# Kernel optimization log

Hardware: AMD Instinct MI355X
Metric: run time of the kernel (lower is better)

The kernel has to match this reference:

```python
import jax, jax.numpy as jnp
import numpy as np

H = 128  # rnn_size

def _run_lstm(x, Wih, Whh, bih, bhh):
    # x: [B, T, D]; Wih: [4H, D]; Whh: [4H, H]; biases: [4H]
    B = x.shape[0]
    xg = jnp.einsum('btd,gd->btg', x, Wih) + bih + bhh  # precompute input projection [B,T,4H]
    WhhT = Whh.T  # [H, 4H]
    def step(carry, xg_t):
        h, c = carry
        g = xg_t + h @ WhhT  # [B, 4H]
        i = jax.nn.sigmoid(g[:, :H])
        f = jax.nn.sigmoid(g[:, H:2 * H])
        gg = jnp.tanh(g[:, 2 * H:3 * H])
        o = jax.nn.sigmoid(g[:, 3 * H:])
        c = f * c + i * gg
        h = o * jnp.tanh(c)
        return (h, c), h
    init = (jnp.zeros((B, H), x.dtype), jnp.zeros((B, H), x.dtype))
    _, ys = jax.lax.scan(step, init, jnp.swapaxes(xg, 0, 1))  # [T, B, H]
    return jnp.swapaxes(ys, 0, 1)  # [B, T, H]

def _bilstm(x, layers):
    h = x
    for (fw, bw) in layers:
        yf = _run_lstm(h, *fw)
        yb = jnp.flip(_run_lstm(jnp.flip(h, axis=1), *bw), axis=1)
        h = jnp.concatenate([yf, yb], axis=-1)  # [B, T, 2H]
    return h

def setup_inputs() -> dict:
    key = jax.random.key(0)
    ks = iter(jax.random.split(key, 32))
    B, T, D = 64, 512, 64
    s = 0.08  # init scale ~ 1/sqrt(H) to avoid gate saturation
    inp = {'x': jax.random.normal(next(ks), (B, T, D), jnp.float32)}
    for name, shape in [
        ('Wih00', (4 * H, D)), ('Whh00', (4 * H, H)), ('bih00', (4 * H,)), ('bhh00', (4 * H,)),
        ('Wih01', (4 * H, D)), ('Whh01', (4 * H, H)), ('bih01', (4 * H,)), ('bhh01', (4 * H,)),
        ('Wih10', (4 * H, 2 * H)), ('Whh10', (4 * H, H)), ('bih10', (4 * H,)), ('bhh10', (4 * H,)),
        ('Wih11', (4 * H, 2 * H)), ('Whh11', (4 * H, H)), ('bih11', (4 * H,)), ('bhh11', (4 * H,)),
        ('W1', (256, 2 * H)), ('b1', (256,)), ('W2', (D, 256)), ('b2', (D,)),
    ]:
        inp[name] = jax.random.normal(next(ks), shape, jnp.float32) * s
    return inp

def reference(x, Wih00, Whh00, bih00, bhh00, Wih01, Whh01, bih01, bhh01,
              Wih10, Whh10, bih10, bhh10, Wih11, Whh11, bih11, bhh11,
              W1, b1, W2, b2):
    layers = [((Wih00, Whh00, bih00, bhh00), (Wih01, Whh01, bih01, bhh01)),
              ((Wih10, Whh10, bih10, bhh10), (Wih11, Whh11, bih11, bhh11))]
    out = _bilstm(x, layers)  # [B, T, 2H]
    h = jax.nn.relu(jnp.einsum('bth,oh->bto', out, W1) + b1)
    return jnp.tanh(jnp.einsum('bth,oh->bto', h, W2) + b2)  # [B, T, input_size]
```

## Files before the change

### kernel.cpp

```cpp
#include <hip/hip_runtime.h>
#include <hip/hip_bf16.h>
#include <hip/hip_fp16.h>

typedef _Float16 h2vec __attribute__((ext_vector_type(2)));
typedef _Float16 f16x8 __attribute__((ext_vector_type(8)));
typedef float f32x4 __attribute__((ext_vector_type(4)));

static __device__ __forceinline__ float fast_sigmoid(float x) {
  return __builtin_amdgcn_rcpf(1.f + __expf(-x));
}
static __device__ __forceinline__ float fast_tanh(float x) {
  return 1.f - 2.f * __builtin_amdgcn_rcpf(__expf(2.f * x) + 1.f);
}
static __device__ __forceinline__ float fdot2u(unsigned int a, unsigned int b, float c) {
#if __has_builtin(__builtin_amdgcn_fdot2)
  return __builtin_amdgcn_fdot2(__builtin_bit_cast(h2vec, a),
                                __builtin_bit_cast(h2vec, b), c, false);
#else
  h2vec av = __builtin_bit_cast(h2vec, a);
  h2vec bv = __builtin_bit_cast(h2vec, b);
  return c + (float)av[0] * (float)bv[0] + (float)av[1] * (float)bv[1];
#endif
}
template<int CTRL>
static __device__ __forceinline__ float dpp_add(float v) {
  int x = __builtin_bit_cast(int, v);
  int y = __builtin_amdgcn_update_dpp(0, x, CTRL, 0xF, 0xF, true);
  return v + __builtin_bit_cast(float, y);
}

template<int MODE>
__global__ __launch_bounds__(256) void gemm_mfma(
    const float* __restrict__ A, const float* __restrict__ W,
    const float* __restrict__ b0, const float* __restrict__ b1,
    float* __restrict__ C, int M, int N, int K) {
  __shared__ __align__(16) unsigned char As[128 * 128];
  __shared__ __align__(16) unsigned char Bs[64 * 128];
  const int tid = threadIdx.x;
  const int wave = tid >> 6, l = tid & 63;
  const int wm = wave >> 1, wn = wave & 1;
  const int m0 = blockIdx.x * 128, n0 = blockIdx.y * 64;
  const int lrow = l & 15, lq = l >> 4;

  f32x4 acc[4][2] = {};

  const int arow = tid >> 1, akc = (tid & 1) * 32;
  const int brow = tid >> 2, bkc = (tid & 3) * 16;

  for (int k0 = 0; k0 < K; k0 += 64) {
    {
      const float* src = A + (size_t)(m0 + arow) * K + k0 + akc;
#pragma unroll
      for (int u = 0; u < 4; ++u) {
        float4 v0 = *reinterpret_cast<const float4*>(src + u * 8);
        float4 v1 = *reinterpret_cast<const float4*>(src + u * 8 + 4);
        f16x8 h;
        h[0] = (_Float16)v0.x; h[1] = (_Float16)v0.y;
        h[2] = (_Float16)v0.z; h[3] = (_Float16)v0.w;
        h[4] = (_Float16)v1.x; h[5] = (_Float16)v1.y;
        h[6] = (_Float16)v1.z; h[7] = (_Float16)v1.w;
        const int kbyte = (akc + u * 8) * 2;
        *reinterpret_cast<f16x8*>(&As[arow * 128 + (kbyte ^ ((arow & 7) << 4))]) = h;
      }
    }
    {
      const float* src = W + (size_t)(n0 + brow) * K + k0 + bkc;
#pragma unroll
      for (int u = 0; u < 2; ++u) {
        float4 v0 = *reinterpret_cast<const float4*>(src + u * 8);
        float4 v1 = *reinterpret_cast<const float4*>(src + u * 8 + 4);
        f16x8 h;
        h[0] = (_Float16)v0.x; h[1] = (_Float16)v0.y;
        h[2] = (_Float16)v0.z; h[3] = (_Float16)v0.w;
        h[4] = (_Float16)v1.x; h[5] = (_Float16)v1.y;
        h[6] = (_Float16)v1.z; h[7] = (_Float16)v1.w;
        const int kbyte = (bkc + u * 8) * 2;
        *reinterpret_cast<f16x8*>(&Bs[brow * 128 + (kbyte ^ ((brow & 7) << 4))]) = h;
      }
    }
    __syncthreads();

#pragma unroll
    for (int kk = 0; kk < 64; kk += 32) {
      const int kbyte = (kk + lq * 8) * 2;
      f16x8 af[4], bf[2];
#pragma unroll
      for (int mt = 0; mt < 4; ++mt) {
        const int row = wm * 64 + mt * 16 + lrow;
        af[mt] = *reinterpret_cast<const f16x8*>(
            &As[row * 128 + (kbyte ^ ((row & 7) << 4))]);
      }
#pragma unroll
      for (int nt = 0; nt < 2; ++nt) {
        const int row = wn * 32 + nt * 16 + lrow;
        bf[nt] = *reinterpret_cast<const f16x8*>(
            &Bs[row * 128 + (kbyte ^ ((row & 7) << 4))]);
      }
#pragma unroll
      for (int mt = 0; mt < 4; ++mt)
#pragma unroll
        for (int nt = 0; nt < 2; ++nt)
          acc[mt][nt] = __builtin_amdgcn_mfma_f32_16x16x32_f16(
              af[mt], bf[nt], acc[mt][nt], 0, 0, 0);
    }
    __syncthreads();
  }

#pragma unroll
  for (int nt = 0; nt < 2; ++nt) {
    const int n = n0 + wn * 32 + nt * 16 + lrow;
    float bias = 0.f;
    if (MODE == 0) bias = b0[n] + b1[n];
    else bias = b0[n];
#pragma unroll
    for (int mt = 0; mt < 4; ++mt) {
#pragma unroll
      for (int r = 0; r < 4; ++r) {
        const int m = m0 + wm * 64 + mt * 16 + lq * 4 + r;
        float val = acc[mt][nt][r] + bias;
        if (MODE == 1) val = fmaxf(val, 0.f);
        if (MODE == 2) val = fast_tanh(val);
        C[(size_t)m * N + n] = val;
      }
    }
  }
}

__global__ __launch_bounds__(256, 1) void lstm_seq2(
    const float* __restrict__ xg_f, const float* __restrict__ xg_b,
    const float* __restrict__ Whh_f, const float* __restrict__ Whh_b,
    float* __restrict__ out) {
  const int b = blockIdx.x;
  const int dir = blockIdx.y;
  const int tid = threadIdx.x;
  const int j2 = tid >> 2;
  const int kq = tid & 3;
  const float* __restrict__ xg  = dir ? xg_b : xg_f;
  const float* __restrict__ Whh = dir ? Whh_b : Whh_f;

  __shared__ unsigned int hbuf[2][80];

  unsigned int w[4][2][16];
#pragma unroll
  for (int g = 0; g < 4; ++g)
#pragma unroll
    for (int u = 0; u < 2; ++u) {
      const float4* wr = reinterpret_cast<const float4*>(
          Whh + (size_t)(g * 128 + 2 * j2 + u) * 128 + kq * 32);
#pragma unroll
      for (int q = 0; q < 8; ++q) {
        float4 v = wr[q];
        __half2 p0 = __floats2half2_rn(v.x, v.y);
        __half2 p1 = __floats2half2_rn(v.z, v.w);
        w[g][u][2 * q]     = __builtin_bit_cast(unsigned int, p0);
        w[g][u][2 * q + 1] = __builtin_bit_cast(unsigned int, p1);
      }
    }

  if (tid < 160) reinterpret_cast<unsigned int*>(hbuf)[tid] = 0u;
  float c0 = 0.f, c1 = 0.f;
  __syncthreads();

  const int tt0 = dir ? 511 : 0;
  const int stp = dir ? -1 : 1;
  const size_t base = (size_t)b * 512 * 512;
  const int xoff = kq * 128 + 2 * j2;
  const bool writer = (kq == (j2 >> 4));
  const int wdst = (j2 >> 4) * 20 + (j2 & 15);

  float2 xv = *reinterpret_cast<const float2*>(xg + base + (size_t)tt0 * 512 + xoff);

  for (int t = 0; t < 512; ++t) {
    const int tt = tt0 + stp * t;

    const unsigned int* hc = &hbuf[t & 1][kq * 20];
    uint4 q0 = reinterpret_cast<const uint4*>(hc)[0];
    uint4 q1 = reinterpret_cast<const uint4*>(hc)[1];
    uint4 q2 = reinterpret_cast<const uint4*>(hc)[2];
    uint4 q3 = reinterpret_cast<const uint4*>(hc)[3];
    unsigned int ha[16];
    ha[0] = q0.x; ha[1] = q0.y; ha[2] = q0.z; ha[3] = q0.w;
    ha[4] = q1.x; ha[5] = q1.y; ha[6] = q1.z; ha[7] = q1.w;
    ha[8] = q2.x; ha[9] = q2.y; ha[10] = q2.z; ha[11] = q2.w;
    ha[12] = q3.x; ha[13] = q3.y; ha[14] = q3.z; ha[15] = q3.w;

    float2 xn = make_float2(0.f, 0.f);
    if (t + 1 < 512)
      xn = *reinterpret_cast<const float2*>(xg + base + (size_t)(tt + stp) * 512 + xoff);

    float acc[4][2];
#pragma unroll
    for (int g = 0; g < 4; ++g) {
      acc[g][0] = (g == kq) ? xv.x : 0.f;
      acc[g][1] = (g == kq) ? xv.y : 0.f;
    }
#pragma unroll
    for (int kk = 0; kk < 16; ++kk) {
#pragma unroll
      for (int g = 0; g < 4; ++g) {
        acc[g][0] = fdot2u(w[g][0][kk], ha[kk], acc[g][0]);
        acc[g][1] = fdot2u(w[g][1][kk], ha[kk], acc[g][1]);
      }
    }
#pragma unroll
    for (int g = 0; g < 4; ++g)
#pragma unroll
      for (int u = 0; u < 2; ++u) {
        float a = acc[g][u];
        a = dpp_add<0xB1>(a);
        a = dpp_add<0x4E>(a);
        acc[g][u] = a;
      }

    const float i0 = fast_sigmoid(acc[0][0]), i1 = fast_sigmoid(acc[0][1]);
    const float f0 = fast_sigmoid(acc[1][0]), f1 = fast_sigmoid(acc[1][1]);
    const float g0 = fast_tanh(acc[2][0]),    g1 = fast_tanh(acc[2][1]);
    const float o0 = fast_sigmoid(acc[3][0]), o1 = fast_sigmoid(acc[3][1]);
    c0 = f0 * c0 + i0 * g0;
    c1 = f1 * c1 + i1 * g1;
    const float h0 = o0 * fast_tanh(c0);
    const float h1 = o1 * fast_tanh(c1);

    if (writer) {
      __half2 hp = __floats2half2_rn(h0, h1);
      hbuf[(t + 1) & 1][wdst] = __builtin_bit_cast(unsigned int, hp);
      *reinterpret_cast<float2*>(out + ((size_t)b * 512 + tt) * 256 + dir * 128 + 2 * j2)
          = make_float2(h0, h1);
    }
    xv = xn;
    __syncthreads();
  }
}

extern "C" void kernel_launch(void* const* d_in, const int* in_sizes, int n_in,
                              void* d_out, int out_size, void* d_ws, size_t ws_size,
                              hipStream_t stream) {
  (void)in_sizes; (void)n_in; (void)out_size; (void)ws_size;

  const float* x     = (const float*)d_in[0];
  const float* Wih00 = (const float*)d_in[1];
  const float* Whh00 = (const float*)d_in[2];
  const float* bih00 = (const float*)d_in[3];
  const float* bhh00 = (const float*)d_in[4];
  const float* Wih01 = (const float*)d_in[5];
  const float* Whh01 = (const float*)d_in[6];
  const float* bih01 = (const float*)d_in[7];
  const float* bhh01 = (const float*)d_in[8];
  const float* Wih10 = (const float*)d_in[9];
  const float* Whh10 = (const float*)d_in[10];
  const float* bih10 = (const float*)d_in[11];
  const float* bhh10 = (const float*)d_in[12];
  const float* Wih11 = (const float*)d_in[13];
  const float* Whh11 = (const float*)d_in[14];
  const float* bih11 = (const float*)d_in[15];
  const float* bhh11 = (const float*)d_in[16];
  const float* W1 = (const float*)d_in[17];
  const float* b1 = (const float*)d_in[18];
  const float* W2 = (const float*)d_in[19];
  const float* b2 = (const float*)d_in[20];
  float* out = (float*)d_out;

  char* ws = (char*)d_ws;
  float* xg_fw = (float*)ws;
  float* xg_bw = (float*)(ws + ((size_t)64 << 20));
  float* buf   = (float*)(ws + ((size_t)128 << 20));

  const int M = 64 * 512;

  gemm_mfma<0><<<dim3(M / 128, 8), 256, 0, stream>>>(
      x, Wih00, bih00, bhh00, xg_fw, M, 512, 64);
  gemm_mfma<0><<<dim3(M / 128, 8), 256, 0, stream>>>(
      x, Wih01, bih01, bhh01, xg_bw, M, 512, 64);
  lstm_seq2<<<dim3(64, 2), 256, 0, stream>>>(xg_fw, xg_bw, Whh00, Whh01, buf);

  gemm_mfma<0><<<dim3(M / 128, 8), 256, 0, stream>>>(
      buf, Wih10, bih10, bhh10, xg_fw, M, 512, 256);
  gemm_mfma<0><<<dim3(M / 128, 8), 256, 0, stream>>>(
      buf, Wih11, bih11, bhh11, xg_bw, M, 512, 256);
  lstm_seq2<<<dim3(64, 2), 256, 0, stream>>>(xg_fw, xg_bw, Whh10, Whh11, buf);

  gemm_mfma<1><<<dim3(M / 128, 4), 256, 0, stream>>>(
      buf, W1, b1, nullptr, xg_fw, M, 256, 256);
  gemm_mfma<2><<<dim3(M / 128, 1), 256, 0, stream>>>(
      xg_fw, W2, b2, nullptr, out, M, 64, 256);
}
```

Baseline: 778.1 us.

## Rework LSTM recurrence to 512 threads, one hidden unit per lane quad

The recurrent kernel now launches 512 threads, one hidden unit per group of four lanes instead of two. Each lane evaluates only one gate nonlinearity, and the four gates are spread across the quad with DPP moves. The time loop is unrolled by two with ping-pong LDS buffers, x-gate prefetch two steps ahead, and a raw s_barrier in place of __syncthreads. This halves the serial per-thread dot-product and activation work per step, at the cost of more waves per barrier and extra cross-lane shuffles.

```diff
diff --git a/kernel.cpp b/kernel.cpp
--- a/kernel.cpp
+++ b/kernel.cpp
@@ -27,6 +27,12 @@
   int x = __builtin_bit_cast(int, v);
   int y = __builtin_amdgcn_update_dpp(0, x, CTRL, 0xF, 0xF, true);
   return v + __builtin_bit_cast(float, y);
+}
+template<int CTRL>
+static __device__ __forceinline__ float dpp_mov(float v) {
+  int x = __builtin_bit_cast(int, v);
+  int y = __builtin_amdgcn_update_dpp(0, x, CTRL, 0xF, 0xF, true);
+  return __builtin_bit_cast(float, y);
 }
 
 template<int MODE>
@@ -126,109 +132,115 @@
   }
 }
 
-__global__ __launch_bounds__(256, 1) void lstm_seq2(
+__global__ __launch_bounds__(512, 2) void lstm_seq5(
     const float* __restrict__ xg_f, const float* __restrict__ xg_b,
     const float* __restrict__ Whh_f, const float* __restrict__ Whh_b,
     float* __restrict__ out) {
   const int b = blockIdx.x;
   const int dir = blockIdx.y;
   const int tid = threadIdx.x;
-  const int j2 = tid >> 2;
+  const int j = tid >> 2;
   const int kq = tid & 3;
   const float* __restrict__ xg  = dir ? xg_b : xg_f;
   const float* __restrict__ Whh = dir ? Whh_b : Whh_f;
 
-  __shared__ unsigned int hbuf[2][80];
-
-  unsigned int w[4][2][16];
-#pragma unroll
-  for (int g = 0; g < 4; ++g)
-#pragma unroll
-    for (int u = 0; u < 2; ++u) {
-      const float4* wr = reinterpret_cast<const float4*>(
-          Whh + (size_t)(g * 128 + 2 * j2 + u) * 128 + kq * 32);
-#pragma unroll
-      for (int q = 0; q < 8; ++q) {
-        float4 v = wr[q];
-        __half2 p0 = __floats2half2_rn(v.x, v.y);
-        __half2 p1 = __floats2half2_rn(v.z, v.w);
-        w[g][u][2 * q]     = __builtin_bit_cast(unsigned int, p0);
-        w[g][u][2 * q + 1] = __builtin_bit_cast(unsigned int, p1);
-      }
-    }
-
-  if (tid < 160) reinterpret_cast<unsigned int*>(hbuf)[tid] = 0u;
-  float c0 = 0.f, c1 = 0.f;
+  __shared__ unsigned int hbuf[2][64];
+
+  unsigned int w[4][16];
+#pragma unroll
+  for (int g = 0; g < 4; ++g) {
+    const float4* wr = reinterpret_cast<const float4*>(
+        Whh + (size_t)(g * 128 + j) * 128 + kq * 32);
+#pragma unroll
+    for (int q = 0; q < 8; ++q) {
+      float4 v = wr[q];
+      __half2 p0 = __floats2half2_rn(v.x, v.y);
+      __half2 p1 = __floats2half2_rn(v.z, v.w);
+      w[g][2 * q]     = __builtin_bit_cast(unsigned int, p0);
+      w[g][2 * q + 1] = __builtin_bit_cast(unsigned int, p1);
+    }
+  }
+
+  if (tid < 128) hbuf[tid >> 6][tid & 63] = 0u;
+  float c = 0.f;
   __syncthreads();
 
   const int tt0 = dir ? 511 : 0;
   const int stp = dir ? -1 : 1;
   const size_t base = (size_t)b * 512 * 512;
-  const int xoff = kq * 128 + 2 * j2;
-  const bool writer = (kq == (j2 >> 4));
-  const int wdst = (j2 >> 4) * 20 + (j2 & 15);
-
-  float2 xv = *reinterpret_cast<const float2*>(xg + base + (size_t)tt0 * 512 + xoff);
-
-  for (int t = 0; t < 512; ++t) {
+  const int xidx = kq * 128 + j;
+
+  float xva = xg[base + (size_t)tt0 * 512 + xidx];
+  float xvb = xg[base + (size_t)(tt0 + stp) * 512 + xidx];
+
+  auto step = [&](int t, unsigned int* rbuf, unsigned int* wbuf, float& xcur)
+      __attribute__((always_inline)) {
     const int tt = tt0 + stp * t;
 
-    const unsigned int* hc = &hbuf[t & 1][kq * 20];
-    uint4 q0 = reinterpret_cast<const uint4*>(hc)[0];
-    uint4 q1 = reinterpret_cast<const uint4*>(hc)[1];
-    uint4 q2 = reinterpret_cast<const uint4*>(hc)[2];
-    uint4 q3 = reinterpret_cast<const uint4*>(hc)[3];
+    const uint4* hc = reinterpret_cast<const uint4*>(&rbuf[kq * 16]);
+    uint4 q0 = hc[0], q1 = hc[1], q2 = hc[2], q3 = hc[3];
     unsigned int ha[16];
     ha[0] = q0.x; ha[1] = q0.y; ha[2] = q0.z; ha[3] = q0.w;
     ha[4] = q1.x; ha[5] = q1.y; ha[6] = q1.z; ha[7] = q1.w;
     ha[8] = q2.x; ha[9] = q2.y; ha[10] = q2.z; ha[11] = q2.w;
     ha[12] = q3.x; ha[13] = q3.y; ha[14] = q3.z; ha[15] = q3.w;
 
-    float2 xn = make_float2(0.f, 0.f);
-    if (t + 1 < 512)
-      xn = *reinterpret_cast<const float2*>(xg + base + (size_t)(tt + stp) * 512 + xoff);
-
-    float acc[4][2];
+    float acc[4] = {0.f, 0.f, 0.f, 0.f};
+#pragma unroll
+    for (int kk = 0; kk < 16; ++kk) {
+#pragma unroll
+      for (int g = 0; g < 4; ++g)
+        acc[g] = fdot2u(w[g][kk], ha[kk], acc[g]);
+    }
+
 #pragma unroll
     for (int g = 0; g < 4; ++g) {
-      acc[g][0] = (g == kq) ? xv.x : 0.f;
-      acc[g][1] = (g == kq) ? xv.y : 0.f;
-    }
-#pragma unroll
-    for (int kk = 0; kk < 16; ++kk) {
-#pragma unroll
-      for (int g = 0; g < 4; ++g) {
-        acc[g][0] = fdot2u(w[g][0][kk], ha[kk], acc[g][0]);
-        acc[g][1] = fdot2u(w[g][1][kk], ha[kk], acc[g][1]);
-      }
-    }
-#pragma unroll
-    for (int g = 0; g < 4; ++g)
-#pragma unroll
-      for (int u = 0; u < 2; ++u) {
-        float a = acc[g][u];
-        a = dpp_add<0xB1>(a);
-        a = dpp_add<0x4E>(a);
-        acc[g][u] = a;
-      }
-
-    const float i0 = fast_sigmoid(acc[0][0]), i1 = fast_sigmoid(acc[0][1]);
-    const float f0 = fast_sigmoid(acc[1][0]), f1 = fast_sigmoid(acc[1][1]);
-    const float g0 = fast_tanh(acc[2][0]),    g1 = fast_tanh(acc[2][1]);
-    const float o0 = fast_sigmoid(acc[3][0]), o1 = fast_sigmoid(acc[3][1]);
-    c0 = f0 * c0 + i0 * g0;
-    c1 = f1 * c1 + i1 * g1;
-    const float h0 = o0 * fast_tanh(c0);
-    const float h1 = o1 * fast_tanh(c1);
-
-    if (writer) {
-      __half2 hp = __floats2half2_rn(h0, h1);
-      hbuf[(t + 1) & 1][wdst] = __builtin_bit_cast(unsigned int, hp);
-      *reinterpret_cast<float2*>(out + ((size_t)b * 512 + tt) * 256 + dir * 128 + 2 * j2)
-          = make_float2(h0, h1);
-    }
-    xv = xn;
-    __syncthreads();
+      float a = acc[g];
+      a = dpp_add<0xB1>(a);
+      a = dpp_add<0x4E>(a);
+      acc[g] = a;
+    }
+
+    float a = acc[0];
+    a = (kq == 1) ? acc[1] : a;
+    a = (kq == 2) ? acc[2] : a;
+    a = (kq == 3) ? acc[3] : a;
+    a += xcur;
+
+    {
+      const int t2 = t + 2;
+      const int tt2 = (t2 < 512) ? (tt0 + stp * t2) : tt0;
+      xcur = xg[base + (size_t)tt2 * 512 + xidx];
+    }
+
+    const float xs = (kq == 2) ? 2.f * a : a;
+    const float y = fast_sigmoid(xs);
+    const float act = (kq == 2) ? 2.f * y - 1.f : y;
+
+    const float gi = dpp_mov<0x00>(act);
+    const float gf = dpp_mov<0x55>(act);
+    const float gg = dpp_mov<0xAA>(act);
+    const float go = dpp_mov<0xFF>(act);
+
+    c = gf * c + gi * gg;
+    const float h = go * (2.f * fast_sigmoid(2.f * c) - 1.f);
+
+    if (kq == 0) {
+      unsigned short us = __builtin_bit_cast(unsigned short, (_Float16)h);
+      reinterpret_cast<unsigned short*>(wbuf)[j] = us;
+    }
+    if (kq == 1) {
+      out[((size_t)b * 512 + tt) * 256 + dir * 128 + j] = h;
+    }
+
+    asm volatile("s_waitcnt lgkmcnt(0)" ::: "memory");
+    __builtin_amdgcn_s_barrier();
+    asm volatile("" ::: "memory");
+  };
+
+  for (int it = 0; it < 256; ++it) {
+    step(2 * it,     hbuf[0], hbuf[1], xva);
+    step(2 * it + 1, hbuf[1], hbuf[0], xvb);
   }
 }
 
@@ -271,13 +283,13 @@
       x, Wih00, bih00, bhh00, xg_fw, M, 512, 64);
   gemm_mfma<0><<<dim3(M / 128, 8), 256, 0, stream>>>(
       x, Wih01, bih01, bhh01, xg_bw, M, 512, 64);
-  lstm_seq2<<<dim3(64, 2), 256, 0, stream>>>(xg_fw, xg_bw, Whh00, Whh01, buf);
+  lstm_seq5<<<dim3(64, 2), 512, 0, stream>>>(xg_fw, xg_bw, Whh00, Whh01, buf);
 
   gemm_mfma<0><<<dim3(M / 128, 8), 256, 0, stream>>>(
       buf, Wih10, bih10, bhh10, xg_fw, M, 512, 256);
   gemm_mfma<0><<<dim3(M / 128, 8), 256, 0, stream>>>(
       buf, Wih11, bih11, bhh11, xg_bw, M, 512, 256);
-  lstm_seq2<<<dim3(64, 2), 256, 0, stream>>>(xg_fw, xg_bw, Whh10, Whh11, buf);
+  lstm_seq5<<<dim3(64, 2), 512, 0, stream>>>(xg_fw, xg_bw, Whh10, Whh11, buf);
 
   gemm_mfma<1><<<dim3(M / 128, 4), 256, 0, stream>>>(
       buf, W1, b1, nullptr, xg_fw, M, 256, 256);
```

Result: faster. 712.1 us (-8.5%).
